# Kernel optimization log

Hardware: AMD Instinct MI355X
Metric: run time of the kernel (lower is better)

Reference implementation:

```python
import jax, jax.numpy as jnp
import numpy as np

B, N, T, C_IN, C_OUT, K, KT = 8, 2048, 64, 32, 64, 3, 3
EPS = 1e-5


def _temporal_conv(x, w, b):
    # x: [B, N, T, Cin] -> Conv1d over time per node.
    b_, n_, t_, cin = x.shape
    x2 = x.reshape(b_ * n_, t_, cin).transpose(0, 2, 1)  # [B*N, Cin, T]
    y = jax.lax.conv_general_dilated(
        x2, w, window_strides=(1,), padding='SAME',
        dimension_numbers=('NCH', 'OIH', 'NCH'))  # [B*N, Cout, T]
    y = y + b[None, :, None]
    # NOTE: the original torch code does reshape (not permute) here, which
    # scrambles the (Cout, T) axes. We faithfully replicate that reshape.
    cout = w.shape[0]
    return y.reshape(b_, n_, t_, cout)


def _cheb_conv(y, L_tilde, cheb_w, cheb_b):
    # y: [B, N, T, C]; Chebyshev recursion over node dim, vectorized over time.
    Tk = [y]
    Tk.append(jnp.einsum('mn,bntc->bmtc', L_tilde, y))
    for k in range(2, K):
        Tk.append(2.0 * jnp.einsum('mn,bntc->bmtc', L_tilde, Tk[k - 1]) - Tk[k - 2])
    Tall = jnp.stack(Tk, axis=0)  # [K, B, N, T, C]
    return jnp.einsum('kbntc,kcd->bntd', Tall, cheb_w) + cheb_b


def setup_inputs() -> dict:
    key = jax.random.key(0)
    ks = jax.random.split(key, 10)
    x = jax.random.normal(ks[0], (B, N, T, C_IN), dtype=jnp.float32)
    # scaled random Laplacian surrogate (spectral norm ~O(1))
    L_tilde = jax.random.normal(ks[1], (N, N), dtype=jnp.float32) / jnp.sqrt(jnp.float32(N))
    s1 = 1.0 / np.sqrt(C_IN * KT)
    w1 = jax.random.normal(ks[2], (C_OUT, C_IN, KT), dtype=jnp.float32) * s1
    b1 = jnp.zeros((C_OUT,), dtype=jnp.float32)
    sc = np.sqrt(6.0 / (C_OUT + C_OUT))  # xavier_uniform over (in,out)
    cheb_w = jax.random.uniform(ks[3], (K, C_OUT, C_OUT), dtype=jnp.float32, minval=-sc, maxval=sc)
    cheb_b = jnp.zeros((C_OUT,), dtype=jnp.float32)
    s2 = 1.0 / np.sqrt(C_OUT * KT)
    w2 = jax.random.normal(ks[4], (C_OUT, C_OUT, KT), dtype=jnp.float32) * s2
    b2 = jnp.zeros((C_OUT,), dtype=jnp.float32)
    gamma = jnp.ones((C_OUT,), dtype=jnp.float32)
    beta = jnp.zeros((C_OUT,), dtype=jnp.float32)
    return {'x': x, 'L_tilde': L_tilde, 'w1': w1, 'b1': b1,
            'cheb_w': cheb_w, 'cheb_b': cheb_b, 'w2': w2, 'b2': b2,
            'gamma': gamma, 'beta': beta}


def reference(x, L_tilde, w1, b1, cheb_w, cheb_b, w2, b2, gamma, beta):
    y = _temporal_conv(x, w1, b1)          # [B, N, T, Cout]
    y = _cheb_conv(y, L_tilde, cheb_w, cheb_b)
    y = _temporal_conv(y, w2, b2)
    # BatchNorm2d (training-mode batch stats) over (B, N, T) per channel.
    mean = jnp.mean(y, axis=(0, 1, 2), keepdims=True)
    var = jnp.var(y, axis=(0, 1, 2), keepdims=True)
    y = (y - mean) * jax.lax.rsqrt(var + EPS) * gamma + beta
    y = jax.nn.relu(y)
    # dropout is identity in eval mode
    return y
```

## Files before the change

kernel.cpp:

```cpp
#include <hip/hip_runtime.h>
#include <cstdint>

typedef __bf16 bf16x8 __attribute__((ext_vector_type(8)));
typedef float floatx4 __attribute__((ext_vector_type(4)));
typedef unsigned int uint4v __attribute__((ext_vector_type(4)));
typedef unsigned int uint2v __attribute__((ext_vector_type(2)));
using u16 = unsigned short;

#define DEVFN static __device__ __forceinline__

#define SZ_BIG   134217728ull
#define OFF_YT   0ull
#define OFF_T1N  0ull
#define OFF_T1T  SZ_BIG
#define OFF_LBF  (2ull*SZ_BIG)
#define OFF_W1SW (OFF_LBF + 8388608ull)
#define OFF_GSW  (OFF_W1SW + 12288ull)
#define OFF_P    (OFF_GSW + 73728ull)
#define OFF_AB   (OFF_P + 1024ull)
#define OFF_S    (OFF_P + 2048ull)
#define OFF_S2   (OFF_S + 1048576ull)

DEVFN u16 f2bf(float f) {
  unsigned u = __builtin_bit_cast(unsigned, f);
  unsigned r = u + 0x7fffu + ((u >> 16) & 1u);
  return (u16)(r >> 16);
}
DEVFN bf16x8 as_bf(uint4v v) { union { uint4v u; bf16x8 b; } x; x.u = v; return x.b; }

DEVFN void gld16(const void* g, void* l) {
  __builtin_amdgcn_global_load_lds(
      (const __attribute__((address_space(1))) void*)(uintptr_t)g,
      (__attribute__((address_space(3))) void*)(unsigned)(uintptr_t)l,
      16, 0, 0);
}

__global__ __launch_bounds__(256) void k_prep1(const float* w1, const float* w2,
                                               const float* chb, char* ws) {
  u16* W1sw = (u16*)(ws + OFF_W1SW);
  float* P  = (float*)(ws + OFF_P);
  int tid = threadIdx.x;
  for (int it = 0; it < 24; ++it) {
    int idx = it * 256 + tid;
    int i = idx & 7, lane = (idx >> 3) & 63, trow = (idx >> 9) & 3, h = idx >> 11;
    int m = trow * 16 + (lane & 15);
    int k = h * 32 + (lane >> 4) * 8 + i;
    W1sw[idx] = f2bf(w1[(m * 32 + (k & 31)) * 3 + (k >> 5)]);
  }
  if (tid < 192) {
    int tp = tid / 3, dt = tid % 3;
    float s = 0.f;
    for (int d = 0; d < 64; ++d) s += w2[(tp * 64 + d) * 3 + dt] * chb[d];
    P[tid] = s;
  }
}

__global__ __launch_bounds__(256) void k_prepG(const float* w2, const float* chw, char* ws) {
  u16* Gsw = (u16*)(ws + OFF_GSW);
  int s = blockIdx.x >> 6, tp = blockIdx.x & 63;
  int tid = threadIdx.x;
  if (tid >= 192) return;
  int dt = tid >> 6, c = tid & 63;
  float acc = 0.f;
  for (int d = 0; d < 64; ++d) {
    float a;
    if (s == 0)      a = chw[(0 * 64 + c) * 64 + d] - chw[(2 * 64 + c) * 64 + d];
    else if (s == 1) a = chw[(1 * 64 + c) * 64 + d];
    else             a = 2.f * chw[(2 * 64 + c) * 64 + d];
    acc += w2[(tp * 64 + d) * 3 + dt] * a;
  }
  int h = tid >> 5, k32 = tid & 31;
  int lane = (k32 >> 3) * 16 + (tp & 15), trow = tp >> 4;
  Gsw[(size_t)(((s * 6 + h) * 4 + trow) * 64 + lane) * 8 + (k32 & 7)] = f2bf(acc);
}

__global__ __launch_bounds__(256) void k_castL(const float* L, char* ws) {
  u16* Lbf = (u16*)(ws + OFF_LBF);
  size_t i = ((size_t)blockIdx.x * 256 + threadIdx.x) * 4;
  float4 v = *(const float4*)(L + i);
  uint2v o;
  o.x = f2bf(v.x) | ((unsigned)f2bf(v.y) << 16);
  o.y = f2bf(v.z) | ((unsigned)f2bf(v.w) << 16);
  *(uint2v*)(Lbf + i) = o;
}

__global__ __launch_bounds__(256) void k_conv1(const float* x, const float* b1, char* ws) {
  __shared__ u16 Wl[6144];
  __shared__ u16 Xt[128 * 104];
  int tid = threadIdx.x, bx = blockIdx.x;
  int nt = bx & 15, ct = (bx >> 4) & 63, b = bx >> 10;
  int n0 = nt * 128;
  const char* wsrc = ws + OFF_W1SW;
  for (int e = 0; e < 3; ++e) {
    int flat = e * 256 + tid;
    gld16(wsrc + flat * 16, (char*)Wl + flat * 16);
  }
  const float* xb = x + ((size_t)(b * 2048 + n0)) * 2048;
  for (int e = 0; e < 12; ++e) {
    int f = e * 256 + tid;
    int nl = f / 24, c4 = f % 24;
    int eo = ct * 32 - 32 + c4 * 4;
    uint2v o = {0u, 0u};
    if (eo >= 0 && eo < 2048) {
      float4 v = *(const float4*)(xb + (size_t)nl * 2048 + eo);
      o.x = f2bf(v.x) | ((unsigned)f2bf(v.y) << 16);
      o.y = f2bf(v.z) | ((unsigned)f2bf(v.w) << 16);
    }
    *(uint2v*)&Xt[nl * 104 + c4 * 4] = o;
  }
  __syncthreads();
  int w = tid >> 6, l = tid & 63, lm = l & 15, q = l >> 4;
  floatx4 zf = {0.f, 0.f, 0.f, 0.f};
  floatx4 acc[4][2];
  for (int s = 0; s < 4; ++s) for (int t = 0; t < 2; ++t) acc[s][t] = zf;
  for (int h = 0; h < 3; ++h) {
    bf16x8 a[4], bb[2];
    for (int s = 0; s < 4; ++s)
      a[s] = as_bf(*(const uint4v*)&Wl[(size_t)((h * 4 + s) * 64 + l) * 8]);
    for (int t = 0; t < 2; ++t) {
      int n = w * 32 + t * 16 + lm;
      bb[t] = as_bf(*(const uint4v*)&Xt[n * 104 + h * 32 + q * 8]);
    }
    for (int s = 0; s < 4; ++s)
      for (int t = 0; t < 2; ++t)
        acc[s][t] = __builtin_amdgcn_mfma_f32_16x16x32_bf16(a[s], bb[t], acc[s][t], 0, 0, 0);
  }
  u16* Yt = (u16*)(ws + OFF_YT);
  for (int s = 0; s < 4; ++s)
    for (int r = 0; r < 4; ++r) {
      int tch = s * 16 + q * 4 + r;
      float bias = b1[tch];
      for (int t = 0; t < 2; ++t) {
        int n = n0 + w * 32 + t * 16 + lm;
        Yt[(size_t)(b * 4096 + tch * 64 + ct) * 2048 + n] = f2bf(acc[s][t][r] + bias);
      }
    }
}

__global__ __launch_bounds__(256) void k_gemm(const char* Pbase, const char* Qbase, char* Cbase,
                                              int MT, size_t P_bs, size_t Q_bs,
                                              size_t C_bs, size_t C_rs) {
  __shared__ u16 Pt[128 * 32];
  __shared__ u16 Qt[128 * 32];
  int tid = threadIdx.x, b = blockIdx.y;
  int rt = blockIdx.x % MT, ctl = blockIdx.x / MT;
  const char* Pp = Pbase + b * P_bs + (size_t)rt * 128 * 4096;
  const char* Qp = Qbase + b * Q_bs + (size_t)ctl * 128 * 4096;
  int w = tid >> 6, l = tid & 63, lm = l & 15, q = l >> 4;
  int wr = (w & 1) * 64, wc = (w >> 1) * 64;
  floatx4 zf = {0.f, 0.f, 0.f, 0.f};
  floatx4 acc[4][4];
  for (int s = 0; s < 4; ++s) for (int t = 0; t < 4; ++t) acc[s][t] = zf;
  for (int k0 = 0; k0 < 2048; k0 += 32) {
    for (int e = 0; e < 2; ++e) {
      int flat = e * 256 + tid;
      int row = flat >> 2, off = (flat & 3) * 16;
      gld16(Pp + (size_t)row * 4096 + k0 * 2 + off, (char*)Pt + flat * 16);
      gld16(Qp + (size_t)row * 4096 + k0 * 2 + off, (char*)Qt + flat * 16);
    }
    __syncthreads();
    bf16x8 a[4], bb[4];
    for (int s = 0; s < 4; ++s) a[s]  = as_bf(*(const uint4v*)&Pt[(wr + s * 16 + lm) * 32 + q * 8]);
    for (int t = 0; t < 4; ++t) bb[t] = as_bf(*(const uint4v*)&Qt[(wc + t * 16 + lm) * 32 + q * 8]);
    for (int s = 0; s < 4; ++s)
      for (int t = 0; t < 4; ++t)
        acc[s][t] = __builtin_amdgcn_mfma_f32_16x16x32_bf16(a[s], bb[t], acc[s][t], 0, 0, 0);
    __syncthreads();
  }
  for (int s = 0; s < 4; ++s)
    for (int r = 0; r < 4; ++r) {
      size_t rg = (size_t)rt * 128 + wr + s * 16 + q * 4 + r;
      char* crow = Cbase + b * C_bs + rg * C_rs;
      for (int t = 0; t < 4; ++t) {
        size_t cg = (size_t)ctl * 128 + wc + t * 16 + lm;
        *(u16*)(crow + cg * 2) = f2bf(acc[s][t][r]);
      }
    }
}

__global__ __launch_bounds__(256) void k_transpose(const char* in, size_t in_bs,
                                                   char* out, size_t out_bs, size_t out_rs) {
  __shared__ u16 LT[64 * 74];
  int tid = threadIdx.x, b = blockIdx.y;
  int jt = blockIdx.x & 63, nt = blockIdx.x >> 6;
  int j0 = jt * 64, n0 = nt * 64;
  for (int e = 0; e < 2; ++e) {
    int flat = e * 256 + tid;
    int jl = flat >> 3, nc = (flat & 7) * 8;
    uint4v v = *(const uint4v*)(in + b * in_bs + (size_t)(j0 + jl) * 4096 + (n0 + nc) * 2);
    u16 u[8] = {(u16)(v.x & 0xffff), (u16)(v.x >> 16), (u16)(v.y & 0xffff), (u16)(v.y >> 16),
                (u16)(v.z & 0xffff), (u16)(v.z >> 16), (u16)(v.w & 0xffff), (u16)(v.w >> 16)};
    for (int i = 0; i < 8; ++i) LT[(nc + i) * 74 + jl] = u[i];
  }
  __syncthreads();
  for (int e = 0; e < 2; ++e) {
    int flat = e * 256 + tid;
    int nl = flat >> 3, jc = (flat & 7) * 8;
    unsigned p[4];
    for (int i = 0; i < 4; ++i) {
      unsigned lo = LT[nl * 74 + jc + 2 * i], hi = LT[nl * 74 + jc + 2 * i + 1];
      p[i] = lo | (hi << 16);
    }
    uint4v v = {p[0], p[1], p[2], p[3]};
    *(uint4v*)(out + b * out_bs + (size_t)(n0 + nl) * out_rs + (j0 + jc) * 2) = v;
  }
}

__global__ __launch_bounds__(256) void k_fused(char* ws, float* dout, const float* b2) {
  __shared__ u16 Gs[12288];
  __shared__ u16 Brow[2][4752];
  int tid = threadIdx.x;
  int np = blockIdx.x, b = blockIdx.y;
  size_t row0 = (size_t)b * 2048 + np * 2;
  if (tid < 144) {
    int r = tid / 72, o = tid % 72;
    Brow[r][o] = 0; Brow[r][65 * 72 + o] = 0;
  }
  int w = tid >> 6, l = tid & 63, lm = l & 15, q = l >> 4;
  int n_loc = w & 1, thalf = w >> 1;
  floatx4 zf = {0.f, 0.f, 0.f, 0.f};
  floatx4 acc[2][4];
  for (int tr = 0; tr < 2; ++tr) for (int tc = 0; tc < 4; ++tc) acc[tr][tc] = zf;
  for (int s = 0; s < 3; ++s) {
    for (int e = 0; e < 6; ++e) {
      int flat = e * 256 + tid;
      gld16(ws + OFF_GSW + (size_t)s * 24576 + flat * 16, (char*)Gs + flat * 16);
    }
    for (int e = 0; e < 4; ++e) {
      int ci = e * 256 + tid;
      int rl = ci >> 9, c = ci & 511;
      size_t rid = row0 + rl;
      const char* src;
      if (s == 0)      src = (const char*)dout + rid * 16384;
      else if (s == 1) src = ws + OFF_T1N + rid * 8192;
      else             src = (const char*)dout + rid * 16384 + 8192;
      uint4v v = *(const uint4v*)(src + c * 16);
      int e0 = 64 + c * 8;
      *(uint4v*)&Brow[rl][(e0 >> 6) * 72 + (e0 & 63)] = v;
    }
    __syncthreads();
    for (int h = 0; h < 6; ++h) {
      int dt = h >> 1, chalf = h & 1;
      bf16x8 a[2], bb[4];
      for (int tr = 0; tr < 2; ++tr)
        a[tr] = as_bf(*(const uint4v*)&Gs[(size_t)((h * 4 + thalf * 2 + tr) * 64 + l) * 8]);
      for (int tc = 0; tc < 4; ++tc) {
        int cp = tc * 16 + lm;
        int ctil = cp + dt;
        bb[tc] = as_bf(*(const uint4v*)&Brow[n_loc][ctil * 72 + chalf * 32 + q * 8]);
      }
      for (int tr = 0; tr < 2; ++tr)
        for (int tc = 0; tc < 4; ++tc)
          acc[tr][tc] = __builtin_amdgcn_mfma_f32_16x16x32_bf16(a[tr], bb[tc], acc[tr][tc], 0, 0, 0);
    }
    __syncthreads();
  }
  const float* P = (const float*)(ws + OFF_P);
  float* orow = dout + (row0 + n_loc) * 4096;
  for (int tr = 0; tr < 2; ++tr)
    for (int r = 0; r < 4; ++r) {
      int tp = thalf * 32 + tr * 16 + q * 4 + r;
      float base = b2[tp] + P[tp * 3 + 1];
      for (int tc = 0; tc < 4; ++tc) {
        int cp = tc * 16 + lm;
        float bias = base + (cp > 0 ? P[tp * 3] : 0.f) + (cp < 63 ? P[tp * 3 + 2] : 0.f);
        orow[tp * 64 + cp] = acc[tr][tc][r] + bias;
      }
    }
}

__global__ __launch_bounds__(256) void k_stats(const float* dout, char* ws) {
  __shared__ float ls[256][8];
  int tid = threadIdx.x;
  size_t base = (size_t)blockIdx.x * 16384 + tid * 4;
  float s0 = 0, s1 = 0, s2 = 0, s3 = 0, t0 = 0, t1 = 0, t2 = 0, t3 = 0;
  for (int it = 0; it < 16; ++it) {
    float4 v = *(const float4*)(dout + base + (size_t)it * 1024);
    s0 += v.x; s1 += v.y; s2 += v.z; s3 += v.w;
    t0 += v.x * v.x; t1 += v.y * v.y; t2 += v.z * v.z; t3 += v.w * v.w;
  }
  ls[tid][0] = s0; ls[tid][1] = s1; ls[tid][2] = s2; ls[tid][3] = s3;
  ls[tid][4] = t0; ls[tid][5] = t1; ls[tid][6] = t2; ls[tid][7] = t3;
  __syncthreads();
  if (tid < 64) {
    int g = tid >> 2, sl = tid & 3;
    float S = 0, S2 = 0;
    for (int j = 0; j < 16; ++j) { S += ls[g + j * 16][sl]; S2 += ls[g + j * 16][4 + sl]; }
    ((float*)(ws + OFF_S))[(size_t)tid * 4096 + blockIdx.x] = S;
    ((float*)(ws + OFF_S2))[(size_t)tid * 4096 + blockIdx.x] = S2;
  }
}

__global__ __launch_bounds__(256) void k_statsf(char* ws, const float* gamma, const float* beta) {
  __shared__ float red[256];
  int c = blockIdx.x, tid = threadIdx.x;
  const float* S  = (const float*)(ws + OFF_S)  + (size_t)c * 4096;
  const float* S2 = (const float*)(ws + OFF_S2) + (size_t)c * 4096;
  float a = 0, bsum = 0;
  for (int j = 0; j < 16; ++j) { a += S[tid + j * 256]; bsum += S2[tid + j * 256]; }
  red[tid] = a; __syncthreads();
  for (int st = 128; st > 0; st >>= 1) { if (tid < st) red[tid] += red[tid + st]; __syncthreads(); }
  float Ssum = red[0]; __syncthreads();
  red[tid] = bsum; __syncthreads();
  for (int st = 128; st > 0; st >>= 1) { if (tid < st) red[tid] += red[tid + st]; __syncthreads(); }
  if (tid == 0) {
    float S2sum = red[0];
    float mean = Ssum / 1048576.f;
    float var = S2sum / 1048576.f - mean * mean;
    float inv = rsqrtf(var + 1e-5f);
    float A = gamma[c] * inv;
    float* AB = (float*)(ws + OFF_AB);
    AB[c] = A; AB[64 + c] = beta[c] - mean * A;
  }
}

__global__ __launch_bounds__(256) void k_bn(float* dout, const char* ws) {
  __shared__ float AB[128];
  int tid = threadIdx.x;
  if (tid < 128) AB[tid] = ((const float*)(ws + OFF_AB))[tid];
  __syncthreads();
  size_t i = ((size_t)blockIdx.x * 256 + tid) * 4;
  int c0 = (tid * 4) & 63;
  float4 v = *(const float4*)(dout + i);
  v.x = fmaxf(0.f, v.x * AB[c0]     + AB[64 + c0]);
  v.y = fmaxf(0.f, v.y * AB[c0 + 1] + AB[64 + c0 + 1]);
  v.z = fmaxf(0.f, v.z * AB[c0 + 2] + AB[64 + c0 + 2]);
  v.w = fmaxf(0.f, v.w * AB[c0 + 3] + AB[64 + c0 + 3]);
  *(float4*)(dout + i) = v;
}

extern "C" void kernel_launch(void* const* d_in, const int* in_sizes, int n_in,
                              void* d_out, int out_size, void* d_ws, size_t ws_size,
                              hipStream_t stream) {
  const float* x   = (const float*)d_in[0];
  const float* L   = (const float*)d_in[1];
  const float* w1  = (const float*)d_in[2];
  const float* b1  = (const float*)d_in[3];
  const float* chw = (const float*)d_in[4];
  const float* chb = (const float*)d_in[5];
  const float* w2  = (const float*)d_in[6];
  const float* b2  = (const float*)d_in[7];
  const float* gam = (const float*)d_in[8];
  const float* bet = (const float*)d_in[9];
  char* ws = (char*)d_ws;
  float* out = (float*)d_out;

  k_prep1<<<1, 256, 0, stream>>>(w1, w2, chb, ws);
  k_prepG<<<192, 256, 0, stream>>>(w2, chw, ws);
  k_castL<<<4096, 256, 0, stream>>>(L, ws);
  k_conv1<<<8192, 256, 0, stream>>>(x, b1, ws);
  k_gemm<<<dim3(512, 8), 256, 0, stream>>>(ws + OFF_YT, ws + OFF_LBF, ws + OFF_T1T,
                                           32, (size_t)16777216, (size_t)0,
                                           (size_t)16777216, (size_t)4096);
  k_gemm<<<dim3(512, 8), 256, 0, stream>>>(ws + OFF_LBF, ws + OFF_T1T, (char*)d_out + 8192,
                                           16, (size_t)0, (size_t)16777216,
                                           (size_t)33554432, (size_t)16384);
  k_transpose<<<dim3(2048, 8), 256, 0, stream>>>(ws + OFF_YT, (size_t)16777216,
                                                 (char*)d_out, (size_t)33554432, (size_t)16384);
  k_transpose<<<dim3(2048, 8), 256, 0, stream>>>(ws + OFF_T1T, (size_t)16777216,
                                                 ws + OFF_T1N, (size_t)16777216, (size_t)8192);
  k_fused<<<dim3(1024, 8), 256, 0, stream>>>(ws, out, b2);
  k_stats<<<4096, 256, 0, stream>>>(out, ws);
  k_statsf<<<64, 256, 0, stream>>>(ws, gam, bet);
  k_bn<<<65536, 256, 0, stream>>>(out, ws);
}
```

Before: 1.527 ms.

## Fuse BN statistics into conv kernel, store bf16 pre-BN, deepen GEMM K-tile with swizzle

The output-conv kernel now computes per-channel sum and sum-of-squares partials in registers and shared memory, then writes the pre-BN activations as bf16 into workspace. This removes the separate stats pass over the fp32 output. The BN kernel reads the bf16 buffer and writes the final fp32 output, so the fp32 intermediate is no longer written and re-read. Separately, the node GEMM now loads 64-wide K tiles with an XOR swizzle to halve barrier count and avoid LDS bank conflicts. Rounding pre-BN values to bf16 adds precision loss, and the bf16 buffer reuses the T1T workspace region.

```diff
diff --git a/kernel.cpp b/kernel.cpp
--- a/kernel.cpp
+++ b/kernel.cpp
@@ -13,13 +13,13 @@
 #define OFF_YT   0ull
 #define OFF_T1N  0ull
 #define OFF_T1T  SZ_BIG
+#define OFF_PB   SZ_BIG
 #define OFF_LBF  (2ull*SZ_BIG)
 #define OFF_W1SW (OFF_LBF + 8388608ull)
 #define OFF_GSW  (OFF_W1SW + 12288ull)
 #define OFF_P    (OFF_GSW + 73728ull)
 #define OFF_AB   (OFF_P + 1024ull)
 #define OFF_S    (OFF_P + 2048ull)
-#define OFF_S2   (OFF_S + 1048576ull)
 
 DEVFN u16 f2bf(float f) {
   unsigned u = __builtin_bit_cast(unsigned, f);
@@ -140,31 +140,36 @@
 __global__ __launch_bounds__(256) void k_gemm(const char* Pbase, const char* Qbase, char* Cbase,
                                               int MT, size_t P_bs, size_t Q_bs,
                                               size_t C_bs, size_t C_rs) {
-  __shared__ u16 Pt[128 * 32];
-  __shared__ u16 Qt[128 * 32];
+  __shared__ u16 Pt[128 * 64];
+  __shared__ u16 Qt[128 * 64];
   int tid = threadIdx.x, b = blockIdx.y;
   int rt = blockIdx.x % MT, ctl = blockIdx.x / MT;
   const char* Pp = Pbase + b * P_bs + (size_t)rt * 128 * 4096;
   const char* Qp = Qbase + b * Q_bs + (size_t)ctl * 128 * 4096;
   int w = tid >> 6, l = tid & 63, lm = l & 15, q = l >> 4;
   int wr = (w & 1) * 64, wc = (w >> 1) * 64;
+  int x7 = lm & 7;
   floatx4 zf = {0.f, 0.f, 0.f, 0.f};
   floatx4 acc[4][4];
   for (int s = 0; s < 4; ++s) for (int t = 0; t < 4; ++t) acc[s][t] = zf;
-  for (int k0 = 0; k0 < 2048; k0 += 32) {
-    for (int e = 0; e < 2; ++e) {
+  for (int k0 = 0; k0 < 2048; k0 += 64) {
+    for (int e = 0; e < 4; ++e) {
       int flat = e * 256 + tid;
-      int row = flat >> 2, off = (flat & 3) * 16;
-      gld16(Pp + (size_t)row * 4096 + k0 * 2 + off, (char*)Pt + flat * 16);
-      gld16(Qp + (size_t)row * 4096 + k0 * 2 + off, (char*)Qt + flat * 16);
+      int row = flat >> 3, c = flat & 7;
+      int sc = c ^ (row & 7);
+      gld16(Pp + (size_t)row * 4096 + k0 * 2 + sc * 16, (char*)Pt + flat * 16);
+      gld16(Qp + (size_t)row * 4096 + k0 * 2 + sc * 16, (char*)Qt + flat * 16);
     }
     __syncthreads();
-    bf16x8 a[4], bb[4];
-    for (int s = 0; s < 4; ++s) a[s]  = as_bf(*(const uint4v*)&Pt[(wr + s * 16 + lm) * 32 + q * 8]);
-    for (int t = 0; t < 4; ++t) bb[t] = as_bf(*(const uint4v*)&Qt[(wc + t * 16 + lm) * 32 + q * 8]);
-    for (int s = 0; s < 4; ++s)
-      for (int t = 0; t < 4; ++t)
-        acc[s][t] = __builtin_amdgcn_mfma_f32_16x16x32_bf16(a[s], bb[t], acc[s][t], 0, 0, 0);
+    for (int ks = 0; ks < 2; ++ks) {
+      int co = ((ks * 4 + q) ^ x7) * 8;
+      bf16x8 a[4], bb[4];
+      for (int s = 0; s < 4; ++s) a[s]  = as_bf(*(const uint4v*)&Pt[(wr + s * 16 + lm) * 64 + co]);
+      for (int t = 0; t < 4; ++t) bb[t] = as_bf(*(const uint4v*)&Qt[(wc + t * 16 + lm) * 64 + co]);
+      for (int s = 0; s < 4; ++s)
+        for (int t = 0; t < 4; ++t)
+          acc[s][t] = __builtin_amdgcn_mfma_f32_16x16x32_bf16(a[s], bb[t], acc[s][t], 0, 0, 0);
+    }
     __syncthreads();
   }
   for (int s = 0; s < 4; ++s)
@@ -206,9 +211,11 @@
   }
 }
 
-__global__ __launch_bounds__(256) void k_fused(char* ws, float* dout, const float* b2) {
+__global__ __launch_bounds__(256) void k_fused(char* ws, const float* dout_src, const float* b2) {
   __shared__ u16 Gs[12288];
   __shared__ u16 Brow[2][4752];
+  __shared__ float SS[4][64][4];
+  __shared__ float SQ[4][64][4];
   int tid = threadIdx.x;
   int np = blockIdx.x, b = blockIdx.y;
   size_t row0 = (size_t)b * 2048 + np * 2;
@@ -231,9 +238,9 @@
       int rl = ci >> 9, c = ci & 511;
       size_t rid = row0 + rl;
       const char* src;
-      if (s == 0)      src = (const char*)dout + rid * 16384;
+      if (s == 0)      src = (const char*)dout_src + rid * 16384;
       else if (s == 1) src = ws + OFF_T1N + rid * 8192;
-      else             src = (const char*)dout + rid * 16384 + 8192;
+      else             src = (const char*)dout_src + rid * 16384 + 8192;
       uint4v v = *(const uint4v*)(src + c * 16);
       int e0 = 64 + c * 8;
       *(uint4v*)&Brow[rl][(e0 >> 6) * 72 + (e0 & 63)] = v;
@@ -256,7 +263,8 @@
     __syncthreads();
   }
   const float* P = (const float*)(ws + OFF_P);
-  float* orow = dout + (row0 + n_loc) * 4096;
+  u16* prow = (u16*)(ws + OFF_PB) + (row0 + n_loc) * 4096;
+  float sloc[4] = {0.f, 0.f, 0.f, 0.f}, sqloc[4] = {0.f, 0.f, 0.f, 0.f};
   for (int tr = 0; tr < 2; ++tr)
     for (int r = 0; r < 4; ++r) {
       int tp = thalf * 32 + tr * 16 + q * 4 + r;
@@ -264,40 +272,31 @@
       for (int tc = 0; tc < 4; ++tc) {
         int cp = tc * 16 + lm;
         float bias = base + (cp > 0 ? P[tp * 3] : 0.f) + (cp < 63 ? P[tp * 3 + 2] : 0.f);
-        orow[tp * 64 + cp] = acc[tr][tc][r] + bias;
+        float v = acc[tr][tc][r] + bias;
+        prow[tp * 64 + cp] = f2bf(v);
+        sloc[tc] += v; sqloc[tc] += v * v;
       }
     }
-}
-
-__global__ __launch_bounds__(256) void k_stats(const float* dout, char* ws) {
-  __shared__ float ls[256][8];
-  int tid = threadIdx.x;
-  size_t base = (size_t)blockIdx.x * 16384 + tid * 4;
-  float s0 = 0, s1 = 0, s2 = 0, s3 = 0, t0 = 0, t1 = 0, t2 = 0, t3 = 0;
-  for (int it = 0; it < 16; ++it) {
-    float4 v = *(const float4*)(dout + base + (size_t)it * 1024);
-    s0 += v.x; s1 += v.y; s2 += v.z; s3 += v.w;
-    t0 += v.x * v.x; t1 += v.y * v.y; t2 += v.z * v.z; t3 += v.w * v.w;
-  }
-  ls[tid][0] = s0; ls[tid][1] = s1; ls[tid][2] = s2; ls[tid][3] = s3;
-  ls[tid][4] = t0; ls[tid][5] = t1; ls[tid][6] = t2; ls[tid][7] = t3;
+  for (int tc = 0; tc < 4; ++tc) { SS[w][l][tc] = sloc[tc]; SQ[w][l][tc] = sqloc[tc]; }
   __syncthreads();
-  if (tid < 64) {
-    int g = tid >> 2, sl = tid & 3;
-    float S = 0, S2 = 0;
-    for (int j = 0; j < 16; ++j) { S += ls[g + j * 16][sl]; S2 += ls[g + j * 16][4 + sl]; }
-    ((float*)(ws + OFF_S))[(size_t)tid * 4096 + blockIdx.x] = S;
-    ((float*)(ws + OFF_S2))[(size_t)tid * 4096 + blockIdx.x] = S2;
+  if (tid < 128) {
+    int c = tid & 63, which = tid >> 6;
+    float s = 0.f;
+    for (int ww = 0; ww < 4; ++ww)
+      for (int qq = 0; qq < 4; ++qq)
+        s += which ? SQ[ww][qq * 16 + (c & 15)][c >> 4] : SS[ww][qq * 16 + (c & 15)][c >> 4];
+    float* Sp = (float*)(ws + OFF_S);
+    Sp[((size_t)which * 64 + c) * 8192 + (size_t)b * 1024 + np] = s;
   }
 }
 
 __global__ __launch_bounds__(256) void k_statsf(char* ws, const float* gamma, const float* beta) {
   __shared__ float red[256];
   int c = blockIdx.x, tid = threadIdx.x;
-  const float* S  = (const float*)(ws + OFF_S)  + (size_t)c * 4096;
-  const float* S2 = (const float*)(ws + OFF_S2) + (size_t)c * 4096;
-  float a = 0, bsum = 0;
-  for (int j = 0; j < 16; ++j) { a += S[tid + j * 256]; bsum += S2[tid + j * 256]; }
+  const float* S  = (const float*)(ws + OFF_S) + (size_t)c * 8192;
+  const float* S2 = S + 64 * 8192;
+  float a = 0.f, bsum = 0.f;
+  for (int j = 0; j < 32; ++j) { a += S[tid + j * 256]; bsum += S2[tid + j * 256]; }
   red[tid] = a; __syncthreads();
   for (int st = 128; st > 0; st >>= 1) { if (tid < st) red[tid] += red[tid + st]; __syncthreads(); }
   float Ssum = red[0]; __syncthreads();
@@ -319,14 +318,27 @@
   int tid = threadIdx.x;
   if (tid < 128) AB[tid] = ((const float*)(ws + OFF_AB))[tid];
   __syncthreads();
-  size_t i = ((size_t)blockIdx.x * 256 + tid) * 4;
-  int c0 = (tid * 4) & 63;
-  float4 v = *(const float4*)(dout + i);
-  v.x = fmaxf(0.f, v.x * AB[c0]     + AB[64 + c0]);
-  v.y = fmaxf(0.f, v.y * AB[c0 + 1] + AB[64 + c0 + 1]);
-  v.z = fmaxf(0.f, v.z * AB[c0 + 2] + AB[64 + c0 + 2]);
-  v.w = fmaxf(0.f, v.w * AB[c0 + 3] + AB[64 + c0 + 3]);
-  *(float4*)(dout + i) = v;
+  const u16* PB = (const u16*)(ws + OFF_PB);
+  size_t i = ((size_t)blockIdx.x * 256 + tid) * 8;
+  int c0 = (int)(i & 63);
+  uint4v v = *(const uint4v*)(PB + i);
+  unsigned uu[4] = {v.x, v.y, v.z, v.w};
+  float f[8];
+  for (int j = 0; j < 4; ++j) {
+    f[2 * j]     = __builtin_bit_cast(float, uu[j] << 16);
+    f[2 * j + 1] = __builtin_bit_cast(float, uu[j] & 0xffff0000u);
+  }
+  float4 o0, o1;
+  o0.x = fmaxf(0.f, f[0] * AB[c0]     + AB[64 + c0]);
+  o0.y = fmaxf(0.f, f[1] * AB[c0 + 1] + AB[64 + c0 + 1]);
+  o0.z = fmaxf(0.f, f[2] * AB[c0 + 2] + AB[64 + c0 + 2]);
+  o0.w = fmaxf(0.f, f[3] * AB[c0 + 3] + AB[64 + c0 + 3]);
+  o1.x = fmaxf(0.f, f[4] * AB[c0 + 4] + AB[64 + c0 + 4]);
+  o1.y = fmaxf(0.f, f[5] * AB[c0 + 5] + AB[64 + c0 + 5]);
+  o1.z = fmaxf(0.f, f[6] * AB[c0 + 6] + AB[64 + c0 + 6]);
+  o1.w = fmaxf(0.f, f[7] * AB[c0 + 7] + AB[64 + c0 + 7]);
+  *(float4*)(dout + i) = o0;
+  *(float4*)(dout + i + 4) = o1;
 }
 
 extern "C" void kernel_launch(void* const* d_in, const int* in_sizes, int n_in,
@@ -359,8 +371,7 @@
                                                  (char*)d_out, (size_t)33554432, (size_t)16384);
   k_transpose<<<dim3(2048, 8), 256, 0, stream>>>(ws + OFF_T1T, (size_t)16777216,
                                                  ws + OFF_T1N, (size_t)16777216, (size_t)8192);
-  k_fused<<<dim3(1024, 8), 256, 0, stream>>>(ws, out, b2);
-  k_stats<<<4096, 256, 0, stream>>>(out, ws);
+  k_fused<<<dim3(1024, 8), 256, 0, stream>>>(ws, (const float*)d_out, b2);
   k_statsf<<<64, 256, 0, stream>>>(ws, gam, bet);
-  k_bn<<<65536, 256, 0, stream>>>(out, ws);
-}
+  k_bn<<<32768, 256, 0, stream>>>(out, ws);
+}
```

After: 1.346 ms. 1.13x faster.
